# Kernel optimization log

Hardware: AMD Instinct MI355X
Metric: run time of the kernel (lower is better)

The kernel has to match this reference:

```python
import jax, jax.numpy as jnp
import numpy as np

HEAD = 4      # args.head
N_HOPS = 2    # n_hops == gt_layer


def setup_inputs() -> dict:
    key = jax.random.key(0)
    ks = jax.random.split(key, 8)
    N, D, E, R = 100000, 64, 800000, 32
    entity_emb = jax.random.normal(ks[0], (N, D), dtype=jnp.float32) * 0.1
    weight = jax.random.normal(ks[1], (R - 1, D), dtype=jnp.float32) * 0.1
    Wq = jax.random.normal(ks[2], (N_HOPS, D, D), dtype=jnp.float32) * (1.0 / np.sqrt(D))
    Wk = jax.random.normal(ks[3], (N_HOPS, D, D), dtype=jnp.float32) * (1.0 / np.sqrt(D))
    Wv = jax.random.normal(ks[4], (N_HOPS, D, D), dtype=jnp.float32) * (1.0 / np.sqrt(D))
    edge_index = jax.random.randint(ks[5], (2, E), 0, N, dtype=jnp.int64 if jax.config.jax_enable_x64 else jnp.int32)
    edge_type = jax.random.randint(ks[6], (E,), 1, R, dtype=edge_index.dtype)  # in [1, R-1]
    return {"entity_emb": entity_emb, "weight": weight, "Wq": Wq, "Wk": Wk,
            "Wv": Wv, "edge_index": edge_index, "edge_type": edge_type}


def _kg_layer(rows, col_embeds, embeds, n_nodes, wq, wk, wv):
    # per-edge scaled-dot attention with index_add softmax normalization
    E, D = col_embeds.shape
    dh = D // HEAD
    q = (embeds[rows] @ wq).reshape(E, HEAD, dh)
    k = (col_embeds @ wk).reshape(E, HEAD, dh)
    v = (col_embeds @ wv).reshape(E, HEAD, dh)
    att = jnp.clip(jnp.einsum('ehd,ehd->eh', q, k), -10.0, 10.0)
    exp_att = jnp.exp(att)                                        # [E, H]
    att_norm = jax.ops.segment_sum(exp_att, rows, num_segments=n_nodes)[rows]
    a = exp_att / (att_norm + 1e-8)
    res = (a[..., None] * v).reshape(E, D)
    return jax.ops.segment_sum(res, rows, num_segments=n_nodes)   # [N, D]


def _scatter_softmax(x, index, n_seg):
    # numerically-stable softmax over edges grouped by index (torch_scatter.scatter_softmax)
    m = jax.ops.segment_max(x, index, num_segments=n_seg)
    e = jnp.exp(x - m[index])
    s = jax.ops.segment_sum(e, index, num_segments=n_seg)
    return e / (s[index] + 1e-16)


def reference(entity_emb, weight, Wq, Wk, Wv, edge_index, edge_type):
    N, D = entity_emb.shape
    head, tail = edge_index[0], edge_index[1]
    rel = weight[edge_type - 1]                                   # [E, D]
    emb = entity_emb
    res = entity_emb
    for layer in range(N_HOPS):
        neigh_rel = emb[tail] * rel                               # [E, D]
        kg_emb = _kg_layer(head, neigh_rel, emb, N, Wq[layer], Wk[layer], Wv[layer])
        # calculate_sim_hrt: product of L2 norms, squared (scalar per edge)
        hn = jnp.linalg.norm(kg_emb[head] * rel, axis=1)
        tn = jnp.linalg.norm(kg_emb[tail] * rel, axis=1)
        w = (hn * tn) ** 2                                        # [E]
        a = _scatter_softmax(w, head, N)                          # [E]
        neigh = a[:, None] * emb[tail]                            # [E, D]
        agg = jax.ops.segment_sum(neigh, head, num_segments=N)    # [N, D]
        # F.normalize + residual accumulation across hops
        emb = agg / jnp.maximum(jnp.linalg.norm(agg, axis=1, keepdims=True), 1e-12)
        res = res + emb
    return res
```

## Files before the change

### kernel.cpp

```cpp
#include <hip/hip_runtime.h>
#include <hip/hip_fp16.h>
#include <math.h>

#define BD 256
#define CAP 192
#define PBLK 2048

#define RED16(v) { v += __shfl_xor(v, 1, 64); v += __shfl_xor(v, 2, 64); \
                   v += __shfl_xor(v, 4, 64); v += __shfl_xor(v, 8, 64); }
#define REDQ(v)  { v += __shfl_xor(v, 16, 64); v += __shfl_xor(v, 32, 64); }

__device__ __forceinline__ __half2 shflxor_h2(__half2 v, int off) {
  int i = __shfl_xor(*(int*)&v, off, 64);
  return *(__half2*)&i;
}
#define REDQH(v)  { v = __hadd2(v, shflxor_h2(v, 16)); v = __hadd2(v, shflxor_h2(v, 32)); }
#define RED16H(v) { v = __hadd2(v, shflxor_h2(v, 1)); v = __hadd2(v, shflxor_h2(v, 2)); \
                    v = __hadd2(v, shflxor_h2(v, 4)); v = __hadd2(v, shflxor_h2(v, 8)); }

__global__ void k_init(const float4* __restrict__ ent, uint2* __restrict__ e16,
                       float4* __restrict__ out, int n4, int* __restrict__ deg, int N) {
  int i = blockIdx.x * BD + threadIdx.x;
  if (i < n4) {
    float4 v = ent[i];
    out[i] = v;
    __half2 h01 = __floats2half2_rn(v.x, v.y);
    __half2 h23 = __floats2half2_rn(v.z, v.w);
    uint2 st; st.x = *(unsigned int*)&h01; st.y = *(unsigned int*)&h23;
    e16[i] = st;
  }
  if (i < N) deg[i] = 0;
}

__global__ void k_deg(const int* __restrict__ head, int* __restrict__ deg, int E) {
  int e = blockIdx.x * BD + threadIdx.x;
  if (e < E) atomicAdd(&deg[head[e]], 1);
}

__global__ void k_scan_a(const int* __restrict__ deg, int* __restrict__ rowptr,
                         int* __restrict__ bsum, int N) {
  __shared__ int s[BD];
  int t = threadIdx.x, i = blockIdx.x * BD + t;
  int v = (i < N) ? deg[i] : 0;
  s[t] = v; __syncthreads();
  for (int off = 1; off < BD; off <<= 1) {
    int add = (t >= off) ? s[t - off] : 0;
    __syncthreads();
    s[t] += add;
    __syncthreads();
  }
  if (i < N) rowptr[i] = s[t] - v;
  if (t == BD - 1) bsum[blockIdx.x] = s[t];
}

__global__ void k_scan_b(const int* __restrict__ bsum, int* __restrict__ boff, int nb) {
  __shared__ int s[512];
  int t = threadIdx.x;
  int v = (t < nb) ? bsum[t] : 0;
  s[t] = v; __syncthreads();
  for (int off = 1; off < 512; off <<= 1) {
    int add = (t >= off) ? s[t - off] : 0;
    __syncthreads();
    s[t] += add;
    __syncthreads();
  }
  boff[t] = s[t] - v;
}

__global__ void k_scan_c(int* __restrict__ rowptr, int* __restrict__ cur,
                         const int* __restrict__ boff, int N, int E) {
  int i = blockIdx.x * BD + threadIdx.x;
  if (i < N) { int v = rowptr[i] + boff[blockIdx.x]; rowptr[i] = v; cur[i] = v; }
  if (i == 0) rowptr[N] = E;
}

__global__ void k_scatter(const int* __restrict__ head, const int* __restrict__ tail,
                          const int* __restrict__ etype,
                          int* __restrict__ cur, int* __restrict__ epk, int E) {
  int e = blockIdx.x * BD + threadIdx.x;
  if (e < E) {
    int p = atomicAdd(&cur[head[e]], 1);
    epk[p] = tail[e] * 32 + (etype[e] - 1);
  }
}

__global__ void k_m(const float* __restrict__ Wq, const float* __restrict__ Wk,
                    const float* __restrict__ weight,
                    float* __restrict__ Mf, __half* __restrict__ w16) {
  int tid = blockIdx.x * BD + threadIdx.x;
  int c = tid & 255;
  int m = tid >> 8;
  int i = c >> 2, h = c & 3;
  const float* wq = Wq + m * 64 + h * 16;
  const float* wk = Wk + i * 64 + h * 16;
  float acc = 0.f;
#pragma unroll
  for (int d = 0; d < 16; d++) acc = fmaf(wq[d], wk[d], acc);
  Mf[tid] = acc;
  if (tid < 2048) {
    int r = tid >> 6, j = tid & 63;
    w16[tid] = __float2half((r < 31) ? weight[r * 64 + j] : 0.f);
  }
}

__global__ __launch_bounds__(256) void k_g(const __half* __restrict__ e16,
                                           const float* __restrict__ Mf,
                                           uint2* __restrict__ Gh2, int N) {
  __shared__ float lM[64 * 256];
  int t = threadIdx.x;
  const float4* Mf4 = (const float4*)Mf;
  float4* lM4 = (float4*)lM;
  for (int i = t; i < 4096; i += BD) lM4[i] = Mf4[i];
  __syncthreads();
  int lane = t & 63, w = t >> 6;
  int nloc0 = blockIdx.x * 64 + w * 16;
#pragma unroll
  for (int b = 0; b < 2; b++) {
    int nl = nloc0 + b * 8;
    float4 acc[8];
#pragma unroll
    for (int ni = 0; ni < 8; ni++) acc[ni] = make_float4(0.f, 0.f, 0.f, 0.f);
#pragma unroll 4
    for (int m = 0; m < 64; m += 2) {
      float4 Mv0 = lM4[m * 64 + lane];
      float4 Mv1 = lM4[(m + 1) * 64 + lane];
#pragma unroll
      for (int ni = 0; ni < 8; ni++) {
        __half2 eh = *(const __half2*)(e16 + (size_t)(nl + ni) * 64 + m);
        float2 ef = __half22float2(eh);
        acc[ni].x = fmaf(ef.x, Mv0.x, acc[ni].x);
        acc[ni].y = fmaf(ef.x, Mv0.y, acc[ni].y);
        acc[ni].z = fmaf(ef.x, Mv0.z, acc[ni].z);
        acc[ni].w = fmaf(ef.x, Mv0.w, acc[ni].w);
        acc[ni].x = fmaf(ef.y, Mv1.x, acc[ni].x);
        acc[ni].y = fmaf(ef.y, Mv1.y, acc[ni].y);
        acc[ni].z = fmaf(ef.y, Mv1.z, acc[ni].z);
        acc[ni].w = fmaf(ef.y, Mv1.w, acc[ni].w);
      }
    }
#pragma unroll
    for (int ni = 0; ni < 8; ni++)
      if (nl + ni < N) {
        __half2 h01 = __floats2half2_rn(acc[ni].x, acc[ni].y);
        __half2 h23 = __floats2half2_rn(acc[ni].z, acc[ni].w);
        uint2 st;
        st.x = *(unsigned int*)&h01;
        st.y = *(unsigned int*)&h23;
        Gh2[(size_t)(nl + ni) * 64 + lane] = st;
      }
  }
}

__global__ __launch_bounds__(256) void k_fused(const uint2* __restrict__ e16,
                        const uint2* __restrict__ w16,
                        const uint4* __restrict__ Ghq, const float* __restrict__ Wv,
                        const int* __restrict__ epk, const int* __restrict__ rowptr,
                        float* __restrict__ kg, int N) {
  __shared__ float SL[4 * 272];
  int t = threadIdx.x, lane = t & 63, w = t >> 6, q = lane >> 4, s = lane & 15;
  float* L = SL + w * 272;
  int wid = blockIdx.x * 4 + w, nw = gridDim.x * 4;
  const __half2 z2 = __float2half2_rn(0.f);
  for (int n = wid; n < N; n += nw) {
    uint4 ga = Ghq[(size_t)n * 32 + s * 2];
    uint4 gb = Ghq[(size_t)n * 32 + s * 2 + 1];
    __half2 c0h01 = *(__half2*)&ga.x, c0h23 = *(__half2*)&ga.y;
    __half2 c1h01 = *(__half2*)&ga.z, c1h23 = *(__half2*)&ga.w;
    __half2 c2h01 = *(__half2*)&gb.x, c2h23 = *(__half2*)&gb.y;
    __half2 c3h01 = *(__half2*)&gb.z, c3h23 = *(__half2*)&gb.w;

    int base = rowptr[n], deg = rowptr[n + 1] - base;
    float4 den = make_float4(0.f, 0.f, 0.f, 0.f);
    __half2 S0a = z2, S0b = z2, S1a = z2, S1b = z2;
    __half2 S2a = z2, S2b = z2, S3a = z2, S3b = z2;
    for (int g0 = 0; g0 < deg; g0 += 4) {
      int k = g0 + q;
      bool valid = (k < deg);
      int kk = min(k, deg - 1);
      int cmb = epk[base + kk];
      uint2 eu = e16[(size_t)(cmb >> 5) * 16 + s];
      uint2 ru = w16[((cmb & 31) << 4) + s];
      __half2 x01 = __hmul2(*(__half2*)&eu.x, *(__half2*)&ru.x);
      __half2 x23 = __hmul2(*(__half2*)&eu.y, *(__half2*)&ru.y);
      __half2 b0 = __low2half2(x01), b1 = __high2half2(x01);
      __half2 b2 = __low2half2(x23), b3 = __high2half2(x23);
      __half2 a01 = __hmul2(b0, c0h01);
      a01 = __hfma2(b1, c1h01, a01);
      a01 = __hfma2(b2, c2h01, a01);
      a01 = __hfma2(b3, c3h01, a01);
      __half2 a23 = __hmul2(b0, c0h23);
      a23 = __hfma2(b1, c1h23, a23);
      a23 = __hfma2(b2, c2h23, a23);
      a23 = __hfma2(b3, c3h23, a23);
      RED16H(a01) RED16H(a23)
      float2 fa01 = __half22float2(a01);
      float2 fa23 = __half22float2(a23);
      fa01.x = fminf(10.f, fmaxf(-10.f, fa01.x));
      fa01.y = fminf(10.f, fmaxf(-10.f, fa01.y));
      fa23.x = fminf(10.f, fmaxf(-10.f, fa23.x));
      fa23.y = fminf(10.f, fmaxf(-10.f, fa23.y));
      float4 ev;
      ev.x = valid ? __expf(fa01.x) : 0.f;
      ev.y = valid ? __expf(fa01.y) : 0.f;
      ev.z = valid ? __expf(fa23.x) : 0.f;
      ev.w = valid ? __expf(fa23.y) : 0.f;
      den.x += ev.x; den.y += ev.y; den.z += ev.z; den.w += ev.w;
      __half2 e01 = __floats2half2_rn(ev.x, ev.y);
      __half2 e23 = __floats2half2_rn(ev.z, ev.w);
      S0a = __hfma2(e01, b0, S0a); S0b = __hfma2(e23, b0, S0b);
      S1a = __hfma2(e01, b1, S1a); S1b = __hfma2(e23, b1, S1b);
      S2a = __hfma2(e01, b2, S2a); S2b = __hfma2(e23, b2, S2b);
      S3a = __hfma2(e01, b3, S3a); S3b = __hfma2(e23, b3, S3b);
    }
    REDQ(den.x) REDQ(den.y) REDQ(den.z) REDQ(den.w)
    REDQH(S0a) REDQH(S0b) REDQH(S1a) REDQH(S1b)
    REDQH(S2a) REDQH(S2b) REDQH(S3a) REDQH(S3b)
    float4 inv;
    inv.x = 1.f / (den.x + 1e-8f); inv.y = 1.f / (den.y + 1e-8f);
    inv.z = 1.f / (den.z + 1e-8f); inv.w = 1.f / (den.w + 1e-8f);
    float2 c0, c1;
    c0 = __half22float2(S0a); c1 = __half22float2(S0b);
    float s0h0 = c0.x * inv.x, s0h1 = c0.y * inv.y, s0h2 = c1.x * inv.z, s0h3 = c1.y * inv.w;
    c0 = __half22float2(S1a); c1 = __half22float2(S1b);
    float s1h0 = c0.x * inv.x, s1h1 = c0.y * inv.y, s1h2 = c1.x * inv.z, s1h3 = c1.y * inv.w;
    c0 = __half22float2(S2a); c1 = __half22float2(S2b);
    float s2h0 = c0.x * inv.x, s2h1 = c0.y * inv.y, s2h2 = c1.x * inv.z, s2h3 = c1.y * inv.w;
    c0 = __half22float2(S3a); c1 = __half22float2(S3b);
    float s3h0 = c0.x * inv.x, s3h1 = c0.y * inv.y, s3h2 = c1.x * inv.z, s3h3 = c1.y * inv.w;
    if (q == 0) {
      *(float4*)(L +       s * 4) = make_float4(s0h0, s1h0, s2h0, s3h0);
      *(float4*)(L +  68 + s * 4) = make_float4(s0h1, s1h1, s2h1, s3h1);
      *(float4*)(L + 136 + s * 4) = make_float4(s0h2, s1h2, s2h2, s3h2);
      *(float4*)(L + 204 + s * 4) = make_float4(s0h3, s1h3, s2h3, s3h3);
    }
    const float4* L4 = (const float4*)(L + q * 68);
    float acc = 0.f;
#pragma unroll
    for (int i4 = 0; i4 < 16; i4++) {
      float4 Lv = L4[i4];
      acc = fmaf(Lv.x, Wv[(i4 * 4 + 0) * 64 + lane], acc);
      acc = fmaf(Lv.y, Wv[(i4 * 4 + 1) * 64 + lane], acc);
      acc = fmaf(Lv.z, Wv[(i4 * 4 + 2) * 64 + lane], acc);
      acc = fmaf(Lv.w, Wv[(i4 * 4 + 3) * 64 + lane], acc);
    }
    kg[(size_t)n * 64 + lane] = acc;
  }
}

__global__ __launch_bounds__(256) void k_d(const float4* __restrict__ kg4,
                    const float* __restrict__ weight,
                    float* __restrict__ D, int N) {
  __shared__ float R2T[64 * 32];
  __shared__ float KG2[64 * 68];
  int t = threadIdx.x;
  for (int i = t; i < 2048; i += BD) {
    int j = i >> 5, r = i & 31;
    float v = (r < 31) ? weight[r * 64 + j] : 0.f;
    R2T[i] = v * v;
  }
  int nbase = blockIdx.x * 64;
  const float4* src = kg4 + (size_t)nbase * 16;
#pragma unroll
  for (int i = 0; i < 4; i++) {
    int idx = t + i * 256;
    float4 v = src[idx];
    float* dst = KG2 + (idx >> 4) * 68 + (idx & 15) * 4;
    dst[0] = v.x * v.x; dst[1] = v.y * v.y; dst[2] = v.z * v.z; dst[3] = v.w * v.w;
  }
  __syncthreads();
  int r = t & 31, ng = t >> 5;
  float acc[8] = {0.f, 0.f, 0.f, 0.f, 0.f, 0.f, 0.f, 0.f};
  const float* kbase = KG2 + ng * 8 * 68;
#pragma unroll 4
  for (int j4 = 0; j4 < 16; j4++) {
    float r0 = R2T[(j4 * 4 + 0) * 32 + r];
    float r1 = R2T[(j4 * 4 + 1) * 32 + r];
    float r2 = R2T[(j4 * 4 + 2) * 32 + r];
    float r3 = R2T[(j4 * 4 + 3) * 32 + r];
#pragma unroll
    for (int ni = 0; ni < 8; ni++) {
      float4 kv = *(const float4*)(kbase + ni * 68 + j4 * 4);
      acc[ni] = fmaf(kv.w, r3, fmaf(kv.z, r2, fmaf(kv.y, r1, fmaf(kv.x, r0, acc[ni]))));
    }
  }
  if (r < 31) {
    int nlim = N - nbase;
#pragma unroll
    for (int ni = 0; ni < 8; ni++) {
      int nl = ng * 8 + ni;
      if (nl < nlim) D[(size_t)(nbase + nl) * 32 + r] = acc[ni];
    }
  }
}

__global__ __launch_bounds__(256) void k_aggnorm(const uint2* __restrict__ e16,
                          const float* __restrict__ D,
                          const int* __restrict__ epk, const int* __restrict__ rowptr,
                          uint2* __restrict__ en16, float* __restrict__ out, int N) {
  __shared__ float wls[4 * CAP];
  __shared__ float DnL[4 * 32];
  int t = threadIdx.x, lane = t & 63, w = t >> 6, q = lane >> 4, s = lane & 15;
  float* wl = wls + w * CAP;
  float* Dn = DnL + w * 32;
  int wid = blockIdx.x * 4 + w, nw = gridDim.x * 4;
  for (int n = wid; n < N; n += nw) {
    int base = rowptr[n], deg = rowptr[n + 1] - base;
    if (lane < 32) Dn[lane] = (lane < 31) ? D[(size_t)n * 32 + lane] : 0.f;
    float4 agg = make_float4(0.f, 0.f, 0.f, 0.f);
    float sacc = 0.f;
    for (int k = lane; k < deg; k += 64) {
      int cmb = epk[base + k];
      float a = __expf(Dn[cmb & 31] * D[cmb]);
      if (k < CAP) wl[k] = a;
      sacc += a;
    }
    RED16(sacc) REDQ(sacc)
    for (int g0 = 0; g0 < deg; g0 += 4) {
      int k = g0 + q;
      bool valid = (k < deg);
      int kk = min(k, deg - 1);
      int cmb = epk[base + kk];
      float a = valid ? ((kk < CAP) ? wl[kk]
                                    : __expf(Dn[cmb & 31] * D[cmb])) : 0.f;
      uint2 eu = e16[(size_t)(cmb >> 5) * 16 + s];
      float2 ef0 = __half22float2(*(__half2*)&eu.x);
      float2 ef1 = __half22float2(*(__half2*)&eu.y);
      agg.x = fmaf(a, ef0.x, agg.x);
      agg.y = fmaf(a, ef0.y, agg.y);
      agg.z = fmaf(a, ef1.x, agg.z);
      agg.w = fmaf(a, ef1.y, agg.w);
    }
    REDQ(agg.x) REDQ(agg.y) REDQ(agg.z) REDQ(agg.w)
    float sinv = 1.f / (sacc + 1e-16f);
    agg.x *= sinv; agg.y *= sinv; agg.z *= sinv; agg.w *= sinv;
    float ss = agg.x * agg.x + agg.y * agg.y + agg.z * agg.z + agg.w * agg.w;
    RED16(ss)
    float nr = fmaxf(sqrtf(ss), 1e-12f);
    float rin = 1.f / nr;
    float4 en;
    en.x = agg.x * rin; en.y = agg.y * rin; en.z = agg.z * rin; en.w = agg.w * rin;
    if (q == 0) {
      __half2 h01 = __floats2half2_rn(en.x, en.y);
      __half2 h23 = __floats2half2_rn(en.z, en.w);
      uint2 st; st.x = *(unsigned int*)&h01; st.y = *(unsigned int*)&h23;
      en16[(size_t)n * 16 + s] = st;
      float4* oo = (float4*)(out + (size_t)n * 64) + s;
      float4 ov = *oo;
      ov.x += en.x; ov.y += en.y; ov.z += en.z; ov.w += en.w;
      *oo = ov;
    }
  }
}

extern "C" void kernel_launch(void* const* d_in, const int* in_sizes, int n_in,
                              void* d_out, int out_size, void* d_ws, size_t ws_size,
                              hipStream_t stream) {
  const float* ent    = (const float*)d_in[0];
  const float* weight = (const float*)d_in[1];
  const float* Wq     = (const float*)d_in[2];
  const float* Wk     = (const float*)d_in[3];
  const float* Wv     = (const float*)d_in[4];
  const int*   eidx   = (const int*)d_in[5];
  const int*   etype  = (const int*)d_in[6];
  int N = in_sizes[0] / 64;
  int E = in_sizes[6];
  const int* head = eidx;
  const int* tail = eidx + E;

  float* ws    = (float*)d_ws;
  size_t o = 0;
  float* e16A  = ws + o; o += (size_t)N * 32;
  float* e16B  = ws + o; o += (size_t)N * 32;
  float* kgbuf = ws + o; o += (size_t)N * 64;
  float* Gbuf  = ws + o; o += (size_t)N * 128;
  float* Mf    = ws + o; o += 64 * 256;
  float* w16   = ws + o; o += 1024;
  int* epk     = (int*)(ws + o); o += (size_t)E;
  int* rowptr  = (int*)(ws + o); o += N + 1;
  int* deg     = (int*)(ws + o); o += N;
  int* cur     = (int*)(ws + o); o += N;
  int* bsum    = (int*)(ws + o); o += 512;
  int* boff    = (int*)(ws + o); o += 512;
  float* Dbuf  = Gbuf;

  int n4  = N * 64 / 4;
  int bl4 = (n4 + BD - 1) / BD;
  int ebl = (E + BD - 1) / BD;
  int sbl = (N + BD - 1) / BD;

  k_init<<<bl4, BD, 0, stream>>>((const float4*)ent, (uint2*)e16A, (float4*)d_out,
                                 n4, deg, N);
  k_deg    <<<ebl, BD, 0, stream>>>(head, deg, E);
  k_scan_a <<<sbl, BD, 0, stream>>>(deg, rowptr, bsum, N);
  k_scan_b <<<1, 512, 0, stream>>>(bsum, boff, sbl);
  k_scan_c <<<sbl, BD, 0, stream>>>(rowptr, cur, boff, N, E);
  k_scatter<<<ebl, BD, 0, stream>>>(head, tail, etype, cur, epk, E);

  float* emb = e16A;
  float* alt = e16B;
  for (int l = 0; l < 2; l++) {
    const float* wq = Wq + (size_t)l * 64 * 64;
    const float* wk = Wk + (size_t)l * 64 * 64;
    const float* wv = Wv + (size_t)l * 64 * 64;

    k_m<<<64, BD, 0, stream>>>(wq, wk, weight, Mf, (__half*)w16);
    k_g<<<(N + 63) / 64, BD, 0, stream>>>((const __half*)emb, Mf, (uint2*)Gbuf, N);
    k_fused<<<PBLK, BD, 0, stream>>>((const uint2*)emb, (const uint2*)w16,
                                     (const uint4*)Gbuf, wv, epk, rowptr, kgbuf, N);
    k_d<<<(N + 63) / 64, BD, 0, stream>>>((const float4*)kgbuf, weight, Dbuf, N);
    k_aggnorm<<<PBLK, BD, 0, stream>>>((const uint2*)emb, Dbuf, epk, rowptr,
                                       (uint2*)alt, (float*)d_out, N);
    float* tmp = emb; emb = alt; alt = tmp;
  }
}
```

Baseline: 577.4 us.

## Split fused attention into edge-parallel logit kernel and node-parallel aggregation

Moves the per-edge attention logit and exp computation out of the per-node loop into a new edge-parallel kernel that writes fp16 exp values per edge, using a new sorted head-index array built in the scatter step. The node-parallel kernel then only reads these precomputed weights and does the weighted sum. This targets load imbalance from variable-degree nodes and wasted lanes on the padded last group. The kg intermediate is also stored as fp16 to halve its traffic. The cost is an extra kernel launch, extra E-sized buffers, a re-gather of G rows per edge instead of once per node, and more fp16 rounding.

```diff
diff --git a/kernel.cpp b/kernel.cpp
--- a/kernel.cpp
+++ b/kernel.cpp
@@ -75,12 +75,14 @@
 }
 
 __global__ void k_scatter(const int* __restrict__ head, const int* __restrict__ tail,
-                          const int* __restrict__ etype,
-                          int* __restrict__ cur, int* __restrict__ epk, int E) {
+                          const int* __restrict__ etype, int* __restrict__ cur,
+                          int* __restrict__ epk, int* __restrict__ hpk, int E) {
   int e = blockIdx.x * BD + threadIdx.x;
   if (e < E) {
-    int p = atomicAdd(&cur[head[e]], 1);
+    int h = head[e];
+    int p = atomicAdd(&cur[h], 1);
     epk[p] = tail[e] * 32 + (etype[e] - 1);
+    hpk[p] = h;
   }
 }
 
@@ -151,24 +153,60 @@
   }
 }
 
-__global__ __launch_bounds__(256) void k_fused(const uint2* __restrict__ e16,
-                        const uint2* __restrict__ w16,
-                        const uint4* __restrict__ Ghq, const float* __restrict__ Wv,
+__global__ __launch_bounds__(256) void k_att(const uint2* __restrict__ e16,
+                        const uint2* __restrict__ w16, const uint4* __restrict__ Ghq,
+                        const int* __restrict__ epk, const int* __restrict__ hpk,
+                        uint2* __restrict__ xat, int E) {
+  int t = threadIdx.x, lane = t & 63, w = t >> 6, q = lane >> 4, s = lane & 15;
+  int wid = blockIdx.x * 4 + w, nw = gridDim.x * 4;
+  int NG = (E + 3) >> 2;
+  for (int g = wid; g < NG; g += nw) {
+    int e = g * 4 + q;
+    int ee = min(e, E - 1);
+    int cmb = epk[ee];
+    int hn  = hpk[ee];
+    uint2 eu = e16[(size_t)(cmb >> 5) * 16 + s];
+    uint2 ru = w16[((cmb & 31) << 4) + s];
+    uint4 ga = Ghq[(size_t)hn * 32 + s * 2];
+    uint4 gb = Ghq[(size_t)hn * 32 + s * 2 + 1];
+    __half2 x01 = __hmul2(*(__half2*)&eu.x, *(__half2*)&ru.x);
+    __half2 x23 = __hmul2(*(__half2*)&eu.y, *(__half2*)&ru.y);
+    __half2 b0 = __low2half2(x01), b1 = __high2half2(x01);
+    __half2 b2 = __low2half2(x23), b3 = __high2half2(x23);
+    __half2 a01 = __hmul2(b0, *(__half2*)&ga.x);
+    a01 = __hfma2(b1, *(__half2*)&ga.z, a01);
+    a01 = __hfma2(b2, *(__half2*)&gb.x, a01);
+    a01 = __hfma2(b3, *(__half2*)&gb.z, a01);
+    __half2 a23 = __hmul2(b0, *(__half2*)&ga.y);
+    a23 = __hfma2(b1, *(__half2*)&ga.w, a23);
+    a23 = __hfma2(b2, *(__half2*)&gb.y, a23);
+    a23 = __hfma2(b3, *(__half2*)&gb.w, a23);
+    RED16H(a01) RED16H(a23)
+    float2 fa01 = __half22float2(a01);
+    float2 fa23 = __half22float2(a23);
+    fa01.x = fminf(10.f, fmaxf(-10.f, fa01.x));
+    fa01.y = fminf(10.f, fmaxf(-10.f, fa01.y));
+    fa23.x = fminf(10.f, fmaxf(-10.f, fa23.x));
+    fa23.y = fminf(10.f, fmaxf(-10.f, fa23.y));
+    if (s == 0 && e < E) {
+      __half2 p01 = __floats2half2_rn(__expf(fa01.x), __expf(fa01.y));
+      __half2 p23 = __floats2half2_rn(__expf(fa23.x), __expf(fa23.y));
+      xat[e] = make_uint2(*(unsigned int*)&p01, *(unsigned int*)&p23);
+    }
+  }
+}
+
+__global__ __launch_bounds__(256) void k_s(const uint2* __restrict__ e16,
+                        const uint2* __restrict__ w16, const uint2* __restrict__ xat,
+                        const float* __restrict__ Wv,
                         const int* __restrict__ epk, const int* __restrict__ rowptr,
-                        float* __restrict__ kg, int N) {
+                        __half* __restrict__ kg16, int N) {
   __shared__ float SL[4 * 272];
   int t = threadIdx.x, lane = t & 63, w = t >> 6, q = lane >> 4, s = lane & 15;
   float* L = SL + w * 272;
   int wid = blockIdx.x * 4 + w, nw = gridDim.x * 4;
   const __half2 z2 = __float2half2_rn(0.f);
   for (int n = wid; n < N; n += nw) {
-    uint4 ga = Ghq[(size_t)n * 32 + s * 2];
-    uint4 gb = Ghq[(size_t)n * 32 + s * 2 + 1];
-    __half2 c0h01 = *(__half2*)&ga.x, c0h23 = *(__half2*)&ga.y;
-    __half2 c1h01 = *(__half2*)&ga.z, c1h23 = *(__half2*)&ga.w;
-    __half2 c2h01 = *(__half2*)&gb.x, c2h23 = *(__half2*)&gb.y;
-    __half2 c3h01 = *(__half2*)&gb.z, c3h23 = *(__half2*)&gb.w;
-
     int base = rowptr[n], deg = rowptr[n + 1] - base;
     float4 den = make_float4(0.f, 0.f, 0.f, 0.f);
     __half2 S0a = z2, S0b = z2, S1a = z2, S1b = z2;
@@ -178,35 +216,18 @@
       bool valid = (k < deg);
       int kk = min(k, deg - 1);
       int cmb = epk[base + kk];
+      uint2 ea = xat[base + kk];
       uint2 eu = e16[(size_t)(cmb >> 5) * 16 + s];
       uint2 ru = w16[((cmb & 31) << 4) + s];
       __half2 x01 = __hmul2(*(__half2*)&eu.x, *(__half2*)&ru.x);
       __half2 x23 = __hmul2(*(__half2*)&eu.y, *(__half2*)&ru.y);
       __half2 b0 = __low2half2(x01), b1 = __high2half2(x01);
       __half2 b2 = __low2half2(x23), b3 = __high2half2(x23);
-      __half2 a01 = __hmul2(b0, c0h01);
-      a01 = __hfma2(b1, c1h01, a01);
-      a01 = __hfma2(b2, c2h01, a01);
-      a01 = __hfma2(b3, c3h01, a01);
-      __half2 a23 = __hmul2(b0, c0h23);
-      a23 = __hfma2(b1, c1h23, a23);
-      a23 = __hfma2(b2, c2h23, a23);
-      a23 = __hfma2(b3, c3h23, a23);
-      RED16H(a01) RED16H(a23)
-      float2 fa01 = __half22float2(a01);
-      float2 fa23 = __half22float2(a23);
-      fa01.x = fminf(10.f, fmaxf(-10.f, fa01.x));
-      fa01.y = fminf(10.f, fmaxf(-10.f, fa01.y));
-      fa23.x = fminf(10.f, fmaxf(-10.f, fa23.x));
-      fa23.y = fminf(10.f, fmaxf(-10.f, fa23.y));
-      float4 ev;
-      ev.x = valid ? __expf(fa01.x) : 0.f;
-      ev.y = valid ? __expf(fa01.y) : 0.f;
-      ev.z = valid ? __expf(fa23.x) : 0.f;
-      ev.w = valid ? __expf(fa23.y) : 0.f;
-      den.x += ev.x; den.y += ev.y; den.z += ev.z; den.w += ev.w;
-      __half2 e01 = __floats2half2_rn(ev.x, ev.y);
-      __half2 e23 = __floats2half2_rn(ev.z, ev.w);
+      __half2 e01 = valid ? *(__half2*)&ea.x : z2;
+      __half2 e23 = valid ? *(__half2*)&ea.y : z2;
+      float2 f0 = __half22float2(e01);
+      float2 f1 = __half22float2(e23);
+      den.x += f0.x; den.y += f0.y; den.z += f1.x; den.w += f1.y;
       S0a = __hfma2(e01, b0, S0a); S0b = __hfma2(e23, b0, S0b);
       S1a = __hfma2(e01, b1, S1a); S1b = __hfma2(e23, b1, S1b);
       S2a = __hfma2(e01, b2, S2a); S2b = __hfma2(e23, b2, S2b);
@@ -243,11 +264,11 @@
       acc = fmaf(Lv.z, Wv[(i4 * 4 + 2) * 64 + lane], acc);
       acc = fmaf(Lv.w, Wv[(i4 * 4 + 3) * 64 + lane], acc);
     }
-    kg[(size_t)n * 64 + lane] = acc;
-  }
-}
-
-__global__ __launch_bounds__(256) void k_d(const float4* __restrict__ kg4,
+    kg16[(size_t)n * 64 + lane] = __float2half(acc);
+  }
+}
+
+__global__ __launch_bounds__(256) void k_d(const uint4* __restrict__ kg16q,
                     const float* __restrict__ weight,
                     float* __restrict__ D, int N) {
   __shared__ float R2T[64 * 32];
@@ -259,13 +280,15 @@
     R2T[i] = v * v;
   }
   int nbase = blockIdx.x * 64;
-  const float4* src = kg4 + (size_t)nbase * 16;
-#pragma unroll
-  for (int i = 0; i < 4; i++) {
-    int idx = t + i * 256;
-    float4 v = src[idx];
-    float* dst = KG2 + (idx >> 4) * 68 + (idx & 15) * 4;
-    dst[0] = v.x * v.x; dst[1] = v.y * v.y; dst[2] = v.z * v.z; dst[3] = v.w * v.w;
+  const uint4* src = kg16q + (size_t)nbase * 8;
+  for (int i = t; i < 512; i += BD) {
+    uint4 v = src[i];
+    float* dst = KG2 + (i >> 3) * 68 + (i & 7) * 8;
+    float2 f;
+    f = __half22float2(*(__half2*)&v.x); dst[0] = f.x * f.x; dst[1] = f.y * f.y;
+    f = __half22float2(*(__half2*)&v.y); dst[2] = f.x * f.x; dst[3] = f.y * f.y;
+    f = __half22float2(*(__half2*)&v.z); dst[4] = f.x * f.x; dst[5] = f.y * f.y;
+    f = __half22float2(*(__half2*)&v.w); dst[6] = f.x * f.x; dst[7] = f.y * f.y;
   }
   __syncthreads();
   int r = t & 31, ng = t >> 5;
@@ -279,8 +302,8 @@
     float r3 = R2T[(j4 * 4 + 3) * 32 + r];
 #pragma unroll
     for (int ni = 0; ni < 8; ni++) {
-      float4 kv = *(const float4*)(kbase + ni * 68 + j4 * 4);
-      acc[ni] = fmaf(kv.w, r3, fmaf(kv.z, r2, fmaf(kv.y, r1, fmaf(kv.x, r0, acc[ni]))));
+      const float* kv = kbase + ni * 68 + j4 * 4;
+      acc[ni] = fmaf(kv[3], r3, fmaf(kv[2], r2, fmaf(kv[1], r1, fmaf(kv[0], r0, acc[ni]))));
     }
   }
   if (r < 31) {
@@ -371,11 +394,13 @@
   size_t o = 0;
   float* e16A  = ws + o; o += (size_t)N * 32;
   float* e16B  = ws + o; o += (size_t)N * 32;
-  float* kgbuf = ws + o; o += (size_t)N * 64;
+  float* kg16  = ws + o; o += (size_t)N * 16;
   float* Gbuf  = ws + o; o += (size_t)N * 128;
   float* Mf    = ws + o; o += 64 * 256;
   float* w16   = ws + o; o += 1024;
   int* epk     = (int*)(ws + o); o += (size_t)E;
+  int* hpk     = (int*)(ws + o); o += (size_t)E;
+  float* xat   = ws + o; o += (size_t)E * 2;
   int* rowptr  = (int*)(ws + o); o += N + 1;
   int* deg     = (int*)(ws + o); o += N;
   int* cur     = (int*)(ws + o); o += N;
@@ -394,7 +419,7 @@
   k_scan_a <<<sbl, BD, 0, stream>>>(deg, rowptr, bsum, N);
   k_scan_b <<<1, 512, 0, stream>>>(bsum, boff, sbl);
   k_scan_c <<<sbl, BD, 0, stream>>>(rowptr, cur, boff, N, E);
-  k_scatter<<<ebl, BD, 0, stream>>>(head, tail, etype, cur, epk, E);
+  k_scatter<<<ebl, BD, 0, stream>>>(head, tail, etype, cur, epk, hpk, E);
 
   float* emb = e16A;
   float* alt = e16B;
@@ -405,9 +430,12 @@
 
     k_m<<<64, BD, 0, stream>>>(wq, wk, weight, Mf, (__half*)w16);
     k_g<<<(N + 63) / 64, BD, 0, stream>>>((const __half*)emb, Mf, (uint2*)Gbuf, N);
-    k_fused<<<PBLK, BD, 0, stream>>>((const uint2*)emb, (const uint2*)w16,
-                                     (const uint4*)Gbuf, wv, epk, rowptr, kgbuf, N);
-    k_d<<<(N + 63) / 64, BD, 0, stream>>>((const float4*)kgbuf, weight, Dbuf, N);
+    k_att<<<PBLK, BD, 0, stream>>>((const uint2*)emb, (const uint2*)w16,
+                                   (const uint4*)Gbuf, epk, hpk, (uint2*)xat, E);
+    k_s<<<PBLK, BD, 0, stream>>>((const uint2*)emb, (const uint2*)w16,
+                                 (const uint2*)xat, wv, epk, rowptr,
+                                 (__half*)kg16, N);
+    k_d<<<(N + 63) / 64, BD, 0, stream>>>((const uint4*)kg16, weight, Dbuf, N);
     k_aggnorm<<<PBLK, BD, 0, stream>>>((const uint2*)emb, Dbuf, epk, rowptr,
                                        (uint2*)alt, (float*)d_out, N);
     float* tmp = emb; emb = alt; alt = tmp;
```

Result: slower. 599.9 us (+3.9%).
